# Kernel tuning notes

Hardware: AMD Instinct MI355X
Metric: run time of the kernel (lower is better)

## Reference

```python
import jax, jax.numpy as jnp
import numpy as np

N_HEAD = 16
D_HEAD = 64
MAX_REL = 512  # max_relative_positions


def setup_inputs() -> dict:
    key = jax.random.key(0)
    ks = jax.random.split(key, 9)
    B, S, D = 2, 2048, 1024
    return {
        "hidden_states": jax.random.normal(ks[0], (B, S, D), jnp.float32),
        "Wq": jax.random.normal(ks[1], (D, D), jnp.float32) * 0.02,
        "bq": jnp.zeros((D,), jnp.float32),
        "Wk": jax.random.normal(ks[2], (D, D), jnp.float32) * 0.02,
        "bk": jnp.zeros((D,), jnp.float32),
        "Wv": jax.random.normal(ks[3], (D, D), jnp.float32) * 0.02,
        "bv": jnp.zeros((D,), jnp.float32),
        "Wc": jax.random.normal(ks[4], (D, D), jnp.float32) * 0.02,
        "pos_table": jax.random.normal(ks[5], (2 * MAX_REL, D_HEAD), jnp.float32) * 0.02,
    }


def reference(hidden_states, Wq, bq, Wk, bk, Wv, bv, Wc, pos_table):
    B, S, D = hidden_states.shape
    H, Dh = N_HEAD, D_HEAD

    # QKV projections (torch Linear: x @ W.T + b)
    q = hidden_states @ Wq.T + bq
    k = hidden_states @ Wk.T + bk
    v = hidden_states @ Wv.T + bv
    q = q.reshape(B, S, H, Dh).transpose(0, 2, 1, 3)  # b h s d
    k = k.reshape(B, S, H, Dh).transpose(0, 2, 1, 3)
    v = v.reshape(B, S, H, Dh).transpose(0, 2, 1, 3)

    # relative position embedding lookup: [S, S, Dh]
    ar = jnp.arange(S)
    rel = jnp.clip(ar[:, None] - ar[None, :] + MAX_REL, 0, 2 * MAX_REL - 1)
    rpe = pos_table[rel]  # (S, S, Dh)

    # c2p: original einsum 'bhld,ijd->bhij' sums q over l (faithful)
    c2p = jnp.einsum('bhld,ijd->bhij', q, rpe)
    p2c = jnp.einsum('bhjd,ijd->bhij', k, jnp.flip(rpe, axis=0))
    bias = c2p + p2c  # (B, H, S, S)

    # SDPA with explicit attn_mask == bias added to scaled scores
    scale = 1.0 / jnp.sqrt(jnp.asarray(Dh, hidden_states.dtype))
    scores = jnp.einsum('bhid,bhjd->bhij', q, k) * scale + bias
    attn = jax.nn.softmax(scores, axis=-1)
    out = jnp.einsum('bhij,bhjd->bhid', attn, v)  # (B, H, S, Dh)

    out = out.transpose(0, 2, 1, 3).reshape(B, S, D)
    return out @ Wc.T  # c_proj has no bias; dropout is identity in eval
```

## Files before the change

kernel.cpp:

```cpp
#include <hip/hip_runtime.h>
#include <math.h>

#define BN   2
#define SEQ  2048
#define DIM  1024
#define NH   16
#define DH   64
#define TAB  1024
#define SCALE 0.125f
#define LOG2E 1.44269504088896340736f

typedef __attribute__((ext_vector_type(8))) short bf16x8;
typedef __attribute__((ext_vector_type(4))) float f32x4;

#if defined(__has_builtin)
#if __has_builtin(__builtin_amdgcn_exp2f)
#define EXP2F(x) __builtin_amdgcn_exp2f(x)
#else
#define EXP2F(x) exp2f(x)
#endif
#else
#define EXP2F(x) exp2f(x)
#endif

__device__ __forceinline__ short f2b(float f) {
    union { float f; unsigned u; } x; x.f = f;
    return (short)((x.u + 0x7fffu + ((x.u >> 16) & 1u)) >> 16);
}
__device__ __forceinline__ float b2f(short s) {
    union { float f; unsigned u; } x; x.u = ((unsigned)(unsigned short)s) << 16;
    return x.f;
}

#define GLDS16(gp, lp) __builtin_amdgcn_global_load_lds( \
    (const __attribute__((address_space(1))) void*)(gp), \
    (__attribute__((address_space(3))) void*)(lp), 16, 0, 0)

__device__ __forceinline__ bf16x8 fragS(const short* base, int row, int kq) {
    return *(const bf16x8*)(base + row * 64 + ((kq ^ (row & 7)) << 3));
}

__global__ __launch_bounds__(256) void f2b_multi_kernel(
    const float* __restrict__ s0, short* __restrict__ d0, int n0,
    const float* __restrict__ s1, short* __restrict__ d1,
    const float* __restrict__ s2, short* __restrict__ d2,
    const float* __restrict__ s3, short* __restrict__ d3, int nw,
    const float* __restrict__ s4, short* __restrict__ d4, int n4)
{
    const int z = blockIdx.z;
    const float* src = z == 0 ? s0 : (z == 1 ? s1 : (z == 2 ? s2 : (z == 3 ? s3 : s4)));
    short* dst       = z == 0 ? d0 : (z == 1 ? d1 : (z == 2 ? d2 : (z == 3 ? d3 : d4)));
    const int n      = z == 0 ? n0 : (z == 4 ? n4 : nw);
    int i = (blockIdx.x * 256 + threadIdx.x) * 8;
    if (i >= n) return;
    float4 a = *(const float4*)&src[i];
    float4 b = *(const float4*)&src[i + 4];
    bf16x8 o = { f2b(a.x), f2b(a.y), f2b(a.z), f2b(a.w),
                 f2b(b.x), f2b(b.y), f2b(b.z), f2b(b.w) };
    *(bf16x8*)&dst[i] = o;
}

__global__ __launch_bounds__(256) void qkv_mfma_kernel(
    const short* __restrict__ xb,
    const short* __restrict__ Wqb, const float* __restrict__ bq,
    const short* __restrict__ Wkb, const float* __restrict__ bk,
    const short* __restrict__ Wvb, const float* __restrict__ bv,
    short* __restrict__ q, short* __restrict__ k, short* __restrict__ v)
{
    const int which = blockIdx.z;
    const short* W    = which == 0 ? Wqb : (which == 1 ? Wkb : Wvb);
    const float* bias = which == 0 ? bq  : (which == 1 ? bk  : bv);
    short* outp       = which == 0 ? q   : (which == 1 ? k   : v);
    const float osc   = which == 0 ? SCALE * LOG2E : 1.0f;

    const int m0 = blockIdx.y * 128;
    const int n0 = blockIdx.x * 128;

    __shared__ short As[128 * 64];
    __shared__ short Bs[128 * 64];

    const int t  = threadIdx.x;
    const int w  = t >> 6;
    const int q4 = (t >> 4) & 3;
    const int l  = t & 15;
    const int wm = (w >> 1) * 64;
    const int wn = (w & 1) * 64;

    f32x4 acc[4][4];
#pragma unroll
    for (int mt = 0; mt < 4; ++mt)
#pragma unroll
        for (int nt = 0; nt < 4; ++nt) acc[mt][nt] = (f32x4){0.f,0.f,0.f,0.f};

    for (int k0 = 0; k0 < DIM; k0 += 64) {
        __syncthreads();
#pragma unroll
        for (int p = 0; p < 4; ++p) {
            const int cq = p * 256 + t;
            const int row = cq >> 3, bd = cq & 7;
            const int goff = (bd ^ (row & 7)) << 3;
            GLDS16(xb + (size_t)(m0 + row) * DIM + k0 + goff, As + cq * 8);
            GLDS16(W  + (size_t)(n0 + row) * DIM + k0 + goff, Bs + cq * 8);
        }
        __syncthreads();
#pragma unroll
        for (int kc = 0; kc < 2; ++kc) {
            bf16x8 af[4], bf[4];
#pragma unroll
            for (int mt = 0; mt < 4; ++mt) af[mt] = fragS(As, wm + mt*16 + l, kc*4 + q4);
#pragma unroll
            for (int nt = 0; nt < 4; ++nt) bf[nt] = fragS(Bs, wn + nt*16 + l, kc*4 + q4);
#pragma unroll
            for (int mt = 0; mt < 4; ++mt)
#pragma unroll
                for (int nt = 0; nt < 4; ++nt)
                    acc[mt][nt] = __builtin_amdgcn_mfma_f32_16x16x32_bf16(
                        af[mt], bf[nt], acc[mt][nt], 0, 0, 0);
        }
    }

    float bv4[4];
#pragma unroll
    for (int nt = 0; nt < 4; ++nt) bv4[nt] = bias[n0 + wn + nt*16 + l];
#pragma unroll
    for (int mt = 0; mt < 4; ++mt) {
#pragma unroll
        for (int r = 0; r < 4; ++r) {
            const int m  = m0 + wm + mt*16 + q4*4 + r;
            const int b_ = m >> 11, s_ = m & 2047;
#pragma unroll
            for (int nt = 0; nt < 4; ++nt) {
                const int o  = n0 + wn + nt*16 + l;
                const int h_ = o >> 6, d_ = o & 63;
                outp[((size_t)(b_*NH + h_) * SEQ + s_) * DH + d_] =
                    f2b((acc[mt][nt][r] + bv4[nt]) * osc);
            }
        }
    }
}

__global__ __launch_bounds__(256) void qsum_c2p_kernel(
    const short* __restrict__ q, const float* __restrict__ pt, float* __restrict__ c2p)
{
    const int bh = blockIdx.x;
    const short* qb = q + (size_t)bh * SEQ * DH;
    __shared__ float part[32][72];
    __shared__ float qs[64];
    const int t = threadIdx.x;
    const int dg = t & 7, sc = t >> 3;
    float a[8];
#pragma unroll
    for (int c = 0; c < 8; ++c) a[c] = 0.f;
    for (int s = sc * 64; s < sc * 64 + 64; ++s) {
        bf16x8 vv = *(const bf16x8*)&qb[(size_t)s * DH + dg * 8];
#pragma unroll
        for (int c = 0; c < 8; ++c) a[c] += b2f(vv[c]);
    }
#pragma unroll
    for (int c = 0; c < 8; ++c) part[sc][dg*8 + c] = a[c];
    __syncthreads();
    if (t < 64) {
        float s = 0.f;
#pragma unroll 8
        for (int i = 0; i < 32; ++i) s += part[i][t];
        qs[t] = s * 8.0f;
    }
    __syncthreads();
    for (int c = t; c < TAB; c += 256) {
        const float* ptr = pt + (size_t)c * DH;
        float s = 0.f;
#pragma unroll
        for (int dd = 0; dd < DH; dd += 4) {
            float4 p4 = *(const float4*)&ptr[dd];
            s += qs[dd]*p4.x + qs[dd+1]*p4.y + qs[dd+2]*p4.z + qs[dd+3]*p4.w;
        }
        c2p[(size_t)bh * TAB + c] = s;
    }
}

__global__ __launch_bounds__(256) void tgemm_kernel(
    const short* __restrict__ kglob, const short* __restrict__ ptb,
    short* __restrict__ slab, int bh0)
{
    const int G    = gridDim.z;
    const int gsub = G >> 3;
    const int fid  = (blockIdx.z * gridDim.y + blockIdx.y) * gridDim.x + blockIdx.x;
    const int g    = (fid & 7) * gsub + ((fid >> 3) % gsub);
    const int rest = fid / (8 * gsub);
    const int m0 = (rest >> 3) * 128;
    const int n0 = (rest & 7) * 128;

    const int bh = bh0 + g;
    const short* A = kglob + (size_t)bh * SEQ * DH;

    __shared__ short As[128 * 64];
    __shared__ short Bs[128 * 64];

    const int t  = threadIdx.x;
    const int w  = t >> 6;
    const int q4 = (t >> 4) & 3;
    const int l  = t & 15;
    const int wm = (w >> 1) * 64;
    const int wn = (w & 1) * 64;

#pragma unroll
    for (int p = 0; p < 4; ++p) {
        const int cq = p * 256 + t;
        const int row = cq >> 3, bd = cq & 7;
        const int go = (bd ^ (row & 7)) << 3;
        GLDS16(A   + (size_t)(m0 + row) * DH + go, As + cq * 8);
        GLDS16(ptb + (size_t)(n0 + row) * DH + go, Bs + cq * 8);
    }
    __syncthreads();

    f32x4 acc[4][4];
#pragma unroll
    for (int mt = 0; mt < 4; ++mt)
#pragma unroll
        for (int nt = 0; nt < 4; ++nt) acc[mt][nt] = (f32x4){0.f,0.f,0.f,0.f};
#pragma unroll
    for (int kc = 0; kc < 2; ++kc) {
        bf16x8 af[4], bf[4];
#pragma unroll
        for (int mt = 0; mt < 4; ++mt) af[mt] = fragS(As, wm + mt*16 + l, kc*4 + q4);
#pragma unroll
        for (int nt = 0; nt < 4; ++nt) bf[nt] = fragS(Bs, wn + nt*16 + l, kc*4 + q4);
#pragma unroll
        for (int mt = 0; mt < 4; ++mt)
#pragma unroll
            for (int nt = 0; nt < 4; ++nt)
                acc[mt][nt] = __builtin_amdgcn_mfma_f32_16x16x32_bf16(
                    af[mt], bf[nt], acc[mt][nt], 0, 0, 0);
    }

    short* outp = slab + (size_t)g * SEQ * 1024;
#pragma unroll
    for (int mt = 0; mt < 4; ++mt)
#pragma unroll
        for (int r = 0; r < 4; ++r) {
            const int m = m0 + wm + mt*16 + q4*4 + r;
#pragma unroll
            for (int nt = 0; nt < 4; ++nt)
                outp[(size_t)m * 1024 + n0 + wn + nt*16 + l] =
                    f2b(acc[mt][nt][r] * LOG2E);
        }
}

__global__ __launch_bounds__(256, 3) void attn_kernel(
    const short* __restrict__ q, const short* __restrict__ k, const short* __restrict__ v,
    const float* __restrict__ c2p, const short* __restrict__ slab,
    short* __restrict__ ao, int bh0)
{
    const int G    = gridDim.y;
    const int gsub = G >> 3;
    const int fid  = blockIdx.y * gridDim.x + blockIdx.x;
    const int g    = (fid & 7) * gsub + ((fid >> 3) % gsub);
    const int i0   = (fid / (8 * gsub)) * 64;

    const int bh = bh0 + g;
    const int b_ = bh >> 4, h_ = bh & 15;
    const short* qbh = q + (size_t)bh * SEQ * DH;
    const short* kbh = k + (size_t)bh * SEQ * DH;
    const short* vbh = v + (size_t)bh * SEQ * DH;
    const float* c2pb = c2p + (size_t)bh * TAB;
    const short* Tb   = slab + (size_t)g * SEQ * 1024;

    __shared__ short QsBand[64 * 72];
    __shared__ short Ks[64 * 64];
    __shared__ short Vt[64 * 64];
    __shared__ float cband[128];
    __shared__ float evf[64];

    const int t    = threadIdx.x;
    const int w    = t >> 6;
    const int q4   = (t >> 4) & 3;
    const int l    = t & 15;
    const int iLoc = w*16 + l;
    const int pq   = ((q4 & 1) << 1) | (q4 >> 1);

#pragma unroll
    for (int p = 0; p < 2; ++p) {
        const int cq = p * 256 + t;
        const int row = cq >> 3, bd = cq & 7;
        GLDS16(qbh + (size_t)(i0 + row) * DH + ((bd ^ (row & 7)) << 3), QsBand + cq * 8);
    }
    __syncthreads();
    const bf16x8 aq0 = fragS(QsBand, w*16 + l, q4);
    const bf16x8 aq1 = fragS(QsBand, w*16 + l, 4 + q4);

    float lsum = 0.f;
    f32x4 O[4];
#pragma unroll
    for (int dt = 0; dt < 4; ++dt) O[dt] = (f32x4){0.f, 0.f, 0.f, 0.f};

    const int jp  = t & 31;
    const int dgv = t >> 5;

    for (int j0 = 0; j0 < SEQ; j0 += 64) {
        const int Kc0 = 2559 - i0 - j0;
        const int cls = (Kc0 >= 1149) ? 0 : (Kc0 <= 0 ? 1 :
                        ((Kc0 >= 126 && Kc0 <= 1023) ? 2 : 3));
        __syncthreads();

#pragma unroll
        for (int p = 0; p < 2; ++p) {
            const int cq = p * 256 + t;
            const int row = cq >> 3, bd = cq & 7;
            GLDS16(kbh + (size_t)(j0 + row) * DH + ((bd ^ (row & 7)) << 3), Ks + cq * 8);
        }
        {
            const int j = 2 * jp, d0 = dgv * 8;
            bf16x8 va = *(const bf16x8*)(vbh + (size_t)(j0 + j)     * DH + d0);
            bf16x8 vb = *(const bf16x8*)(vbh + (size_t)(j0 + j + 1) * DH + d0);
#pragma unroll
            for (int c = 0; c < 8; ++c) {
                const int d = d0 + c;
                const int slot = d * 64 + (((j >> 3) ^ (d & 7)) << 3) + (j & 7);
                short2 pr; pr.x = va[c]; pr.y = vb[c];
                *(short2*)&Vt[slot] = pr;
            }
        }
        if (cls <= 1) {
            if (t < 64)
                evf[t] = b2f(Tb[(size_t)(j0 + t) * 1024 + (cls == 0 ? 1023 : 0)]);
        } else {
            const int rowj = t >> 2, m0b = t & 3;
            const int tb = Kc0 - rowj;
            const int af = min(max((tb - 63) & ~7, 0), 952);
            const short* srcrow = Tb + (size_t)(j0 + rowj) * 1024 + af;
            short* dstrow = &QsBand[rowj * 72];
            *(int4*)&dstrow[m0b * 8]       = *(const int4*)&srcrow[m0b * 8];
            *(int4*)&dstrow[(m0b + 4) * 8] = *(const int4*)&srcrow[(m0b + 4) * 8];
            if (m0b == 0)
                *(int4*)&dstrow[64] = *(const int4*)&srcrow[64];
        }
        if (t < 128) {
            int cc = min(max(449 + i0 - j0 + t, 0), TAB - 1);
            cband[t] = c2pb[cc];
        }
        __syncthreads();

        f32x4 st4[4];
        const int cb0 = iLoc - q4*4 + 63;
#pragma unroll
        for (int jt = 0; jt < 4; ++jt) {
            const int base = cb0 - jt*16;
            st4[jt][0] = cband[base];
            st4[jt][1] = cband[base - 1];
            st4[jt][2] = cband[base - 2];
            st4[jt][3] = cband[base - 3];
        }
        if (cls <= 1) {
#pragma unroll
            for (int jt = 0; jt < 4; ++jt) {
                const float4 e4 = *(const float4*)&evf[jt*16 + q4*4];
                st4[jt][0] += e4.x; st4[jt][1] += e4.y;
                st4[jt][2] += e4.z; st4[jt][3] += e4.w;
            }
        }

        __builtin_amdgcn_s_setprio(1);
#pragma unroll
        for (int jt = 0; jt < 4; ++jt) {
            bf16x8 a0 = fragS(Ks, jt*16 + l, q4);
            bf16x8 a1 = fragS(Ks, jt*16 + l, 4 + q4);
            st4[jt] = __builtin_amdgcn_mfma_f32_16x16x32_bf16(a0, aq0, st4[jt], 0, 0, 0);
            st4[jt] = __builtin_amdgcn_mfma_f32_16x16x32_bf16(a1, aq1, st4[jt], 0, 0, 0);
        }
        __builtin_amdgcn_s_setprio(0);

        float pv4[4][4];
        if (cls <= 1) {
#pragma unroll
            for (int jt = 0; jt < 4; ++jt)
#pragma unroll
                for (int r = 0; r < 4; ++r)
                    pv4[jt][r] = EXP2F(st4[jt][r]);
        } else if (cls == 2) {
#pragma unroll
            for (int jt = 0; jt < 4; ++jt)
#pragma unroll
                for (int r = 0; r < 4; ++r) {
                    const int jl = jt*16 + q4*4 + r;
                    const int tb = Kc0 - jl;
                    const int af = min((tb - 63) & ~7, 952);
                    pv4[jt][r] = EXP2F(st4[jt][r] +
                                       b2f(QsBand[jl * 72 + (tb - iLoc - af)]));
                }
        } else {
#pragma unroll
            for (int jt = 0; jt < 4; ++jt)
#pragma unroll
                for (int r = 0; r < 4; ++r) {
                    const int jl = jt*16 + q4*4 + r;
                    const int tb = Kc0 - jl;
                    const int af = min(max((tb - 63) & ~7, 0), 952);
                    const int y  = min(max(tb - iLoc, 0), 1023);
                    pv4[jt][r] = EXP2F(st4[jt][r] +
                                       b2f(QsBand[jl * 72 + (y - af)]));
                }
        }
#pragma unroll
        for (int jt = 0; jt < 4; ++jt)
#pragma unroll
            for (int r = 0; r < 4; ++r) lsum += pv4[jt][r];

        unsigned P2[4][2];
#pragma unroll
        for (int t2 = 0; t2 < 4; ++t2) {
            asm("v_cvt_pk_bf16_f32 %0, %1, %2"
                : "=v"(P2[t2][0]) : "v"(pv4[t2][0]), "v"(pv4[t2][1]));
            asm("v_cvt_pk_bf16_f32 %0, %1, %2"
                : "=v"(P2[t2][1]) : "v"(pv4[t2][2]), "v"(pv4[t2][3]));
        }
#pragma unroll
        for (int m = 0; m < 2; ++m) {
            asm("v_permlane16_swap_b32 %0, %1" : "+v"(P2[0][m]), "+v"(P2[1][m]));
            asm("v_permlane16_swap_b32 %0, %1" : "+v"(P2[2][m]), "+v"(P2[3][m]));
        }
        union { unsigned u[4]; bf16x8 v8; } UA, UB;
        UA.u[0] = P2[0][0]; UA.u[1] = P2[0][1]; UA.u[2] = P2[1][0]; UA.u[3] = P2[1][1];
        UB.u[0] = P2[2][0]; UB.u[1] = P2[2][1]; UB.u[2] = P2[3][0]; UB.u[3] = P2[3][1];

        __builtin_amdgcn_s_setprio(1);
#pragma unroll
        for (int dt = 0; dt < 4; ++dt) {
            bf16x8 b0 = fragS(Vt, dt*16 + l, pq);
            bf16x8 b1 = fragS(Vt, dt*16 + l, 4 + pq);
            O[dt] = __builtin_amdgcn_mfma_f32_16x16x32_bf16(UA.v8, b0, O[dt], 0, 0, 0);
            O[dt] = __builtin_amdgcn_mfma_f32_16x16x32_bf16(UB.v8, b1, O[dt], 0, 0, 0);
        }
        __builtin_amdgcn_s_setprio(0);
    }

    lsum += __shfl_xor(lsum, 16);
    lsum += __shfl_xor(lsum, 32);

#pragma unroll
    for (int r = 0; r < 4; ++r) {
        const float inv = 1.f / __shfl(lsum, q4*4 + r);
        const int i_g = i0 + w*16 + q4*4 + r;
        short* dst = ao + (((size_t)b_ * SEQ + i_g) * NH + h_) * DH + l;
#pragma unroll
        for (int dt = 0; dt < 4; ++dt)
            dst[dt*16] = f2b(O[dt][r] * inv);
    }
}

__global__ __launch_bounds__(256) void out_mfma_kernel(
    const short* __restrict__ xb, const float* __restrict__ W, float* __restrict__ out)
{
    const int m0 = blockIdx.y * 128;
    const int n0 = blockIdx.x * 128;

    __shared__ short As[128 * 64];
    __shared__ short Bs[128 * 64];

    const int t  = threadIdx.x;
    const int w  = t >> 6;
    const int q4 = (t >> 4) & 3;
    const int l  = t & 15;
    const int wm = (w >> 1) * 64;
    const int wn = (w & 1) * 64;

    f32x4 acc[4][4];
#pragma unroll
    for (int mt = 0; mt < 4; ++mt)
#pragma unroll
        for (int nt = 0; nt < 4; ++nt) acc[mt][nt] = (f32x4){0.f,0.f,0.f,0.f};

    for (int k0 = 0; k0 < DIM; k0 += 64) {
        __syncthreads();
#pragma unroll
        for (int p = 0; p < 4; ++p) {
            const int cq = p * 256 + t;
            const int row = cq >> 3, bd = cq & 7;
            GLDS16(xb + (size_t)(m0 + row) * DIM + k0 + ((bd ^ (row & 7)) << 3), As + cq * 8);
        }
        {
            const int row = t >> 1, h = t & 1;
#pragma unroll
            for (int c = 0; c < 4; ++c) {
                const int gch = h * 4 + c;
                const float* src = W + (size_t)(n0 + row) * DIM + k0 + gch * 8;
                float4 f0 = *(const float4*)src;
                float4 f1 = *(const float4*)(src + 4);
                bf16x8 o = { f2b(f0.x), f2b(f0.y), f2b(f0.z), f2b(f0.w),
                             f2b(f1.x), f2b(f1.y), f2b(f1.z), f2b(f1.w) };
                *(bf16x8*)&Bs[row * 64 + ((gch ^ (row & 7)) << 3)] = o;
            }
        }
        __syncthreads();
#pragma unroll
        for (int kc = 0; kc < 2; ++kc) {
            bf16x8 af[4], bf[4];
#pragma unroll
            for (int mt = 0; mt < 4; ++mt) af[mt] = fragS(As, wm + mt*16 + l, kc*4 + q4);
#pragma unroll
            for (int nt = 0; nt < 4; ++nt) bf[nt] = fragS(Bs, wn + nt*16 + l, kc*4 + q4);
#pragma unroll
            for (int mt = 0; mt < 4; ++mt)
#pragma unroll
                for (int nt = 0; nt < 4; ++nt)
                    acc[mt][nt] = __builtin_amdgcn_mfma_f32_16x16x32_bf16(
                        af[mt], bf[nt], acc[mt][nt], 0, 0, 0);
        }
    }
#pragma unroll
    for (int mt = 0; mt < 4; ++mt)
#pragma unroll
        for (int r = 0; r < 4; ++r) {
            const int m = m0 + wm + mt*16 + q4*4 + r;
#pragma unroll
            for (int nt = 0; nt < 4; ++nt)
                out[(size_t)m * DIM + n0 + wn + nt*16 + l] = acc[mt][nt][r];
        }
}

extern "C" void kernel_launch(void* const* d_in, const int* in_sizes, int n_in,
                              void* d_out, int out_size, void* d_ws, size_t ws_size,
                              hipStream_t stream)
{
    const float* hs = (const float*)d_in[0];
    const float* Wq = (const float*)d_in[1];
    const float* bq = (const float*)d_in[2];
    const float* Wk = (const float*)d_in[3];
    const float* bk = (const float*)d_in[4];
    const float* Wv = (const float*)d_in[5];
    const float* bv = (const float*)d_in[6];
    const float* Wc = (const float*)d_in[7];
    const float* pt = (const float*)d_in[8];
    float* out = (float*)d_out;

    const size_t XE    = (size_t)BN * SEQ * DIM;
    const size_t WE    = (size_t)DIM * DIM;
    const size_t PE    = (size_t)TAB * DH;
    const size_t SLAB1 = (size_t)SEQ * 1024;

    short* sw   = (short*)d_ws;
    short* qb   = sw;
    short* kb   = sw + XE;
    short* vb   = sw + 2 * XE;
    short* aob  = sw + 3 * XE;
    float* c2p  = (float*)(sw + 4 * XE);
    short* ptb  = sw + 4 * XE + 65536;
    short* slab = sw + 4 * XE + 65536 + PE;
    short* xb   = slab;
    short* wqb  = slab + XE;
    short* wkb  = wqb + WE;
    short* wvb  = wkb + WE;

    const size_t fixed_sh = 4 * XE + 65536 + PE;
    const size_t avail_sh = (ws_size / 2 > fixed_sh) ? ws_size / 2 - fixed_sh : 0;
    const int G = (avail_sh >= 32 * SLAB1) ? 32 : ((avail_sh >= 16 * SLAB1) ? 16 : 8);

    f2b_multi_kernel<<<dim3((int)(XE/2048), 1, 5), 256, 0, stream>>>(
        hs, xb, (int)XE, Wq, wqb, Wk, wkb, Wv, wvb, (int)WE, pt, ptb, (int)PE);

    qkv_mfma_kernel<<<dim3(DIM/128, (BN*SEQ)/128, 3), 256, 0, stream>>>(
        xb, wqb, bq, wkb, bk, wvb, bv, qb, kb, vb);

    qsum_c2p_kernel<<<dim3(BN*NH), 256, 0, stream>>>(qb, pt, c2p);

    for (int bh0 = 0; bh0 < BN*NH; bh0 += G) {
        tgemm_kernel<<<dim3(1024/128, SEQ/128, G), 256, 0, stream>>>(kb, ptb, slab, bh0);
        attn_kernel<<<dim3(SEQ/64, G), 256, 0, stream>>>(qb, kb, vb, c2p, slab, aob, bh0);
    }

    out_mfma_kernel<<<dim3(DIM/128, (BN*SEQ)/128), 256, 0, stream>>>(aob, Wc, out);
}
```

Baseline: 341.2 us.

## Double-buffer K, V, bias band and c2p tiles in the attention loop

The attention kernel gets ping-pong LDS buffers for K, the transposed V, the relative-position band, the c2p band and the edge values. The next tile's global loads are issued into registers, or straight into LDS via GLDS16, before computing on the current tile, and are written to the other buffer after the PV MFMAs. This drops one barrier per iteration and is meant to hide global-load latency behind the MFMA and exp work. In exchange it roughly doubles LDS use and holds more live registers, which may reduce occupancy.

```diff
diff --git a/kernel.cpp b/kernel.cpp
--- a/kernel.cpp
+++ b/kernel.cpp
@@ -265,11 +265,12 @@
     const float* c2pb = c2p + (size_t)bh * TAB;
     const short* Tb   = slab + (size_t)g * SEQ * 1024;
 
-    __shared__ short QsBand[64 * 72];
-    __shared__ short Ks[64 * 64];
-    __shared__ short Vt[64 * 64];
-    __shared__ float cband[128];
-    __shared__ float evf[64];
+    __shared__ short BandA[64 * 72];
+    __shared__ short BandB[64 * 72];
+    __shared__ short KsA[64 * 64], KsB[64 * 64];
+    __shared__ short VtA[64 * 64], VtB[64 * 64];
+    __shared__ float cbA[128], cbB[128];
+    __shared__ float evA[64], evB[64];
 
     const int t    = threadIdx.x;
     const int w    = t >> 6;
@@ -278,82 +279,140 @@
     const int iLoc = w*16 + l;
     const int pq   = ((q4 & 1) << 1) | (q4 >> 1);
 
+    const int jp  = t & 31;
+    const int dgv = t >> 5;
+    const int rowj = t >> 2, m0b = t & 3;
+
 #pragma unroll
     for (int p = 0; p < 2; ++p) {
         const int cq = p * 256 + t;
         const int row = cq >> 3, bd = cq & 7;
-        GLDS16(qbh + (size_t)(i0 + row) * DH + ((bd ^ (row & 7)) << 3), QsBand + cq * 8);
+        GLDS16(qbh + (size_t)(i0 + row) * DH + ((bd ^ (row & 7)) << 3), BandA + cq * 8);
     }
     __syncthreads();
-    const bf16x8 aq0 = fragS(QsBand, w*16 + l, q4);
-    const bf16x8 aq1 = fragS(QsBand, w*16 + l, 4 + q4);
-
-    float lsum = 0.f;
-    f32x4 O[4];
-#pragma unroll
-    for (int dt = 0; dt < 4; ++dt) O[dt] = (f32x4){0.f, 0.f, 0.f, 0.f};
-
-    const int jp  = t & 31;
-    const int dgv = t >> 5;
-
-    for (int j0 = 0; j0 < SEQ; j0 += 64) {
-        const int Kc0 = 2559 - i0 - j0;
-        const int cls = (Kc0 >= 1149) ? 0 : (Kc0 <= 0 ? 1 :
-                        ((Kc0 >= 126 && Kc0 <= 1023) ? 2 : 3));
-        __syncthreads();
-
+    const bf16x8 aq0 = fragS(BandA, w*16 + l, q4);
+    const bf16x8 aq1 = fragS(BandA, w*16 + l, 4 + q4);
+    __syncthreads();
+
+    {
+        const int j0n = 0;
+        const int Kc0n = 2559 - i0;
+        const int clsn = (Kc0n >= 1149) ? 0 : (Kc0n <= 0 ? 1 :
+                         ((Kc0n >= 126 && Kc0n <= 1023) ? 2 : 3));
 #pragma unroll
         for (int p = 0; p < 2; ++p) {
             const int cq = p * 256 + t;
             const int row = cq >> 3, bd = cq & 7;
-            GLDS16(kbh + (size_t)(j0 + row) * DH + ((bd ^ (row & 7)) << 3), Ks + cq * 8);
+            GLDS16(kbh + (size_t)(j0n + row) * DH + ((bd ^ (row & 7)) << 3), KsA + cq * 8);
         }
         {
-            const int j = 2 * jp, d0 = dgv * 8;
-            bf16x8 va = *(const bf16x8*)(vbh + (size_t)(j0 + j)     * DH + d0);
-            bf16x8 vb = *(const bf16x8*)(vbh + (size_t)(j0 + j + 1) * DH + d0);
+            const int jv = 2 * jp, d0v = dgv * 8;
+            bf16x8 va = *(const bf16x8*)(vbh + (size_t)(j0n + jv)     * DH + d0v);
+            bf16x8 vb = *(const bf16x8*)(vbh + (size_t)(j0n + jv + 1) * DH + d0v);
 #pragma unroll
             for (int c = 0; c < 8; ++c) {
-                const int d = d0 + c;
-                const int slot = d * 64 + (((j >> 3) ^ (d & 7)) << 3) + (j & 7);
+                const int d = d0v + c;
+                const int slot = d * 64 + (((jv >> 3) ^ (d & 7)) << 3) + (jv & 7);
                 short2 pr; pr.x = va[c]; pr.y = vb[c];
-                *(short2*)&Vt[slot] = pr;
-            }
-        }
-        if (cls <= 1) {
+                *(short2*)&VtA[slot] = pr;
+            }
+        }
+        if (clsn <= 1) {
             if (t < 64)
-                evf[t] = b2f(Tb[(size_t)(j0 + t) * 1024 + (cls == 0 ? 1023 : 0)]);
+                evA[t] = b2f(Tb[(size_t)(j0n + t) * 1024 + (clsn == 0 ? 1023 : 0)]);
         } else {
-            const int rowj = t >> 2, m0b = t & 3;
-            const int tb = Kc0 - rowj;
+            const int tb = Kc0n - rowj;
             const int af = min(max((tb - 63) & ~7, 0), 952);
-            const short* srcrow = Tb + (size_t)(j0 + rowj) * 1024 + af;
-            short* dstrow = &QsBand[rowj * 72];
+            const short* srcrow = Tb + (size_t)(j0n + rowj) * 1024 + af;
+            short* dstrow = &BandA[rowj * 72];
             *(int4*)&dstrow[m0b * 8]       = *(const int4*)&srcrow[m0b * 8];
             *(int4*)&dstrow[(m0b + 4) * 8] = *(const int4*)&srcrow[(m0b + 4) * 8];
             if (m0b == 0)
                 *(int4*)&dstrow[64] = *(const int4*)&srcrow[64];
         }
         if (t < 128) {
-            int cc = min(max(449 + i0 - j0 + t, 0), TAB - 1);
-            cband[t] = c2pb[cc];
-        }
-        __syncthreads();
+            int cc = min(max(449 + i0 - j0n + t, 0), TAB - 1);
+            cbA[t] = c2pb[cc];
+        }
+    }
+    __syncthreads();
+
+    float lsum = 0.f;
+    f32x4 O[4];
+#pragma unroll
+    for (int dt = 0; dt < 4; ++dt) O[dt] = (f32x4){0.f, 0.f, 0.f, 0.f};
+
+    for (int it = 0; it < 32; ++it) {
+        const int j0  = it * 64;
+        const int par = it & 1;
+        const short* KsC   = par ? KsB   : KsA;
+        const short* VtC   = par ? VtB   : VtA;
+        const short* BandC = par ? BandB : BandA;
+        const float* cbC   = par ? cbB   : cbA;
+        const float* evC   = par ? evB   : evA;
+        short* KsN   = par ? KsA   : KsB;
+        short* VtN   = par ? VtA   : VtB;
+        short* BandN = par ? BandA : BandB;
+        float* cbN   = par ? cbA   : cbB;
+        float* evN   = par ? evA   : evB;
+
+        const int Kc0 = 2559 - i0 - j0;
+        const int cls = (Kc0 >= 1149) ? 0 : (Kc0 <= 0 ? 1 :
+                        ((Kc0 >= 126 && Kc0 <= 1023) ? 2 : 3));
+
+        const bool have_nxt = (it < 31);
+        const int j0n  = j0 + 64;
+        const int Kc0n = Kc0 - 64;
+        const int clsn = (Kc0n >= 1149) ? 0 : (Kc0n <= 0 ? 1 :
+                         ((Kc0n >= 126 && Kc0n <= 1023) ? 2 : 3));
+
+        bf16x8 va = {}, vb = {};
+        int4 bl0 = {}, bl1 = {}, bl2 = {};
+        float cbv = 0.f, evv = 0.f;
+        int afn = 0;
+        if (have_nxt) {
+#pragma unroll
+            for (int p = 0; p < 2; ++p) {
+                const int cq = p * 256 + t;
+                const int row = cq >> 3, bd = cq & 7;
+                GLDS16(kbh + (size_t)(j0n + row) * DH + ((bd ^ (row & 7)) << 3), KsN + cq * 8);
+            }
+            {
+                const int jv = 2 * jp, d0v = dgv * 8;
+                va = *(const bf16x8*)(vbh + (size_t)(j0n + jv)     * DH + d0v);
+                vb = *(const bf16x8*)(vbh + (size_t)(j0n + jv + 1) * DH + d0v);
+            }
+            if (clsn <= 1) {
+                if (t < 64)
+                    evv = b2f(Tb[(size_t)(j0n + t) * 1024 + (clsn == 0 ? 1023 : 0)]);
+            } else {
+                const int tb = Kc0n - rowj;
+                afn = min(max((tb - 63) & ~7, 0), 952);
+                const short* srcrow = Tb + (size_t)(j0n + rowj) * 1024 + afn;
+                bl0 = *(const int4*)&srcrow[m0b * 8];
+                bl1 = *(const int4*)&srcrow[(m0b + 4) * 8];
+                if (m0b == 0) bl2 = *(const int4*)&srcrow[64];
+            }
+            if (t < 128) {
+                int cc = min(max(449 + i0 - j0n + t, 0), TAB - 1);
+                cbv = c2pb[cc];
+            }
+        }
 
         f32x4 st4[4];
         const int cb0 = iLoc - q4*4 + 63;
 #pragma unroll
         for (int jt = 0; jt < 4; ++jt) {
             const int base = cb0 - jt*16;
-            st4[jt][0] = cband[base];
-            st4[jt][1] = cband[base - 1];
-            st4[jt][2] = cband[base - 2];
-            st4[jt][3] = cband[base - 3];
+            st4[jt][0] = cbC[base];
+            st4[jt][1] = cbC[base - 1];
+            st4[jt][2] = cbC[base - 2];
+            st4[jt][3] = cbC[base - 3];
         }
         if (cls <= 1) {
 #pragma unroll
             for (int jt = 0; jt < 4; ++jt) {
-                const float4 e4 = *(const float4*)&evf[jt*16 + q4*4];
+                const float4 e4 = *(const float4*)&evC[jt*16 + q4*4];
                 st4[jt][0] += e4.x; st4[jt][1] += e4.y;
                 st4[jt][2] += e4.z; st4[jt][3] += e4.w;
             }
@@ -362,8 +421,8 @@
         __builtin_amdgcn_s_setprio(1);
 #pragma unroll
         for (int jt = 0; jt < 4; ++jt) {
-            bf16x8 a0 = fragS(Ks, jt*16 + l, q4);
-            bf16x8 a1 = fragS(Ks, jt*16 + l, 4 + q4);
+            bf16x8 a0 = fragS(KsC, jt*16 + l, q4);
+            bf16x8 a1 = fragS(KsC, jt*16 + l, 4 + q4);
             st4[jt] = __builtin_amdgcn_mfma_f32_16x16x32_bf16(a0, aq0, st4[jt], 0, 0, 0);
             st4[jt] = __builtin_amdgcn_mfma_f32_16x16x32_bf16(a1, aq1, st4[jt], 0, 0, 0);
         }
@@ -385,7 +444,7 @@
                     const int tb = Kc0 - jl;
                     const int af = min((tb - 63) & ~7, 952);
                     pv4[jt][r] = EXP2F(st4[jt][r] +
-                                       b2f(QsBand[jl * 72 + (tb - iLoc - af)]));
+                                       b2f(BandC[jl * 72 + (tb - iLoc - af)]));
                 }
         } else {
 #pragma unroll
@@ -397,7 +456,7 @@
                     const int af = min(max((tb - 63) & ~7, 0), 952);
                     const int y  = min(max(tb - iLoc, 0), 1023);
                     pv4[jt][r] = EXP2F(st4[jt][r] +
-                                       b2f(QsBand[jl * 72 + (y - af)]));
+                                       b2f(BandC[jl * 72 + (y - af)]));
                 }
         }
 #pragma unroll
@@ -425,12 +484,35 @@
         __builtin_amdgcn_s_setprio(1);
 #pragma unroll
         for (int dt = 0; dt < 4; ++dt) {
-            bf16x8 b0 = fragS(Vt, dt*16 + l, pq);
-            bf16x8 b1 = fragS(Vt, dt*16 + l, 4 + pq);
+            bf16x8 b0 = fragS(VtC, dt*16 + l, pq);
+            bf16x8 b1 = fragS(VtC, dt*16 + l, 4 + pq);
             O[dt] = __builtin_amdgcn_mfma_f32_16x16x32_bf16(UA.v8, b0, O[dt], 0, 0, 0);
             O[dt] = __builtin_amdgcn_mfma_f32_16x16x32_bf16(UB.v8, b1, O[dt], 0, 0, 0);
         }
         __builtin_amdgcn_s_setprio(0);
+
+        if (have_nxt) {
+            {
+                const int jv = 2 * jp, d0v = dgv * 8;
+#pragma unroll
+                for (int c = 0; c < 8; ++c) {
+                    const int d = d0v + c;
+                    const int slot = d * 64 + (((jv >> 3) ^ (d & 7)) << 3) + (jv & 7);
+                    short2 pr; pr.x = va[c]; pr.y = vb[c];
+                    *(short2*)&VtN[slot] = pr;
+                }
+            }
+            if (clsn <= 1) {
+                if (t < 64) evN[t] = evv;
+            } else {
+                short* dstrow = &BandN[rowj * 72];
+                *(int4*)&dstrow[m0b * 8]       = bl0;
+                *(int4*)&dstrow[(m0b + 4) * 8] = bl1;
+                if (m0b == 0) *(int4*)&dstrow[64] = bl2;
+            }
+            if (t < 128) cbN[t] = cbv;
+        }
+        __syncthreads();
     }
 
     lsum += __shfl_xor(lsum, 16);
```

New measurement: 350.8 us. +2.8%, slower.

## Read bias band and c2p directly from global instead of staging in LDS

Applied to the files above, without the earlier changes.

Drops the LDS staging of the positional slab band, the c2p band and the edge vector, along with the per-tile case classification. Each thread now gathers its 16 bias terms straight from global memory with clamped indices, and Q is staged through the K buffer to save LDS. The intent is to cut LDS footprint, barriers and branch divergence. In exchange it issues scattered, uncoalesced 2-byte global loads with a stride of a 2KB row per element, which adds latency inside the main loop.

```diff
diff --git a/kernel.cpp b/kernel.cpp
--- a/kernel.cpp
+++ b/kernel.cpp
@@ -265,11 +265,8 @@
     const float* c2pb = c2p + (size_t)bh * TAB;
     const short* Tb   = slab + (size_t)g * SEQ * 1024;
 
-    __shared__ short QsBand[64 * 72];
     __shared__ short Ks[64 * 64];
     __shared__ short Vt[64 * 64];
-    __shared__ float cband[128];
-    __shared__ float evf[64];
 
     const int t    = threadIdx.x;
     const int w    = t >> 6;
@@ -278,29 +275,27 @@
     const int iLoc = w*16 + l;
     const int pq   = ((q4 & 1) << 1) | (q4 >> 1);
 
+    const int jp  = t & 31;
+    const int dgv = t >> 5;
+
 #pragma unroll
     for (int p = 0; p < 2; ++p) {
         const int cq = p * 256 + t;
         const int row = cq >> 3, bd = cq & 7;
-        GLDS16(qbh + (size_t)(i0 + row) * DH + ((bd ^ (row & 7)) << 3), QsBand + cq * 8);
+        GLDS16(qbh + (size_t)(i0 + row) * DH + ((bd ^ (row & 7)) << 3), Ks + cq * 8);
     }
     __syncthreads();
-    const bf16x8 aq0 = fragS(QsBand, w*16 + l, q4);
-    const bf16x8 aq1 = fragS(QsBand, w*16 + l, 4 + q4);
+    const bf16x8 aq0 = fragS(Ks, w*16 + l, q4);
+    const bf16x8 aq1 = fragS(Ks, w*16 + l, 4 + q4);
+    __syncthreads();
 
     float lsum = 0.f;
     f32x4 O[4];
 #pragma unroll
     for (int dt = 0; dt < 4; ++dt) O[dt] = (f32x4){0.f, 0.f, 0.f, 0.f};
 
-    const int jp  = t & 31;
-    const int dgv = t >> 5;
-
     for (int j0 = 0; j0 < SEQ; j0 += 64) {
         const int Kc0 = 2559 - i0 - j0;
-        const int cls = (Kc0 >= 1149) ? 0 : (Kc0 <= 0 ? 1 :
-                        ((Kc0 >= 126 && Kc0 <= 1023) ? 2 : 3));
-        __syncthreads();
 
 #pragma unroll
         for (int p = 0; p < 2; ++p) {
@@ -320,44 +315,27 @@
                 *(short2*)&Vt[slot] = pr;
             }
         }
-        if (cls <= 1) {
-            if (t < 64)
-                evf[t] = b2f(Tb[(size_t)(j0 + t) * 1024 + (cls == 0 ? 1023 : 0)]);
-        } else {
-            const int rowj = t >> 2, m0b = t & 3;
-            const int tb = Kc0 - rowj;
-            const int af = min(max((tb - 63) & ~7, 0), 952);
-            const short* srcrow = Tb + (size_t)(j0 + rowj) * 1024 + af;
-            short* dstrow = &QsBand[rowj * 72];
-            *(int4*)&dstrow[m0b * 8]       = *(const int4*)&srcrow[m0b * 8];
-            *(int4*)&dstrow[(m0b + 4) * 8] = *(const int4*)&srcrow[(m0b + 4) * 8];
-            if (m0b == 0)
-                *(int4*)&dstrow[64] = *(const int4*)&srcrow[64];
-        }
-        if (t < 128) {
-            int cc = min(max(449 + i0 - j0 + t, 0), TAB - 1);
-            cband[t] = c2pb[cc];
-        }
         __syncthreads();
 
         f32x4 st4[4];
-        const int cb0 = iLoc - q4*4 + 63;
-#pragma unroll
-        for (int jt = 0; jt < 4; ++jt) {
-            const int base = cb0 - jt*16;
-            st4[jt][0] = cband[base];
-            st4[jt][1] = cband[base - 1];
-            st4[jt][2] = cband[base - 2];
-            st4[jt][3] = cband[base - 3];
-        }
-        if (cls <= 1) {
-#pragma unroll
-            for (int jt = 0; jt < 4; ++jt) {
-                const float4 e4 = *(const float4*)&evf[jt*16 + q4*4];
-                st4[jt][0] += e4.x; st4[jt][1] += e4.y;
-                st4[jt][2] += e4.z; st4[jt][3] += e4.w;
+        const int ccb = 512 + i0 + iLoc - j0;
+#pragma unroll
+        for (int jt = 0; jt < 4; ++jt)
+#pragma unroll
+            for (int r = 0; r < 4; ++r) {
+                const int jl = jt*16 + q4*4 + r;
+                st4[jt][r] = c2pb[min(max(ccb - jl, 0), TAB - 1)];
             }
-        }
+
+        short tband[16];
+#pragma unroll
+        for (int jt = 0; jt < 4; ++jt)
+#pragma unroll
+            for (int r = 0; r < 4; ++r) {
+                const int jl = jt*16 + q4*4 + r;
+                const int y  = min(max(Kc0 - jl - iLoc, 0), TAB - 1);
+                tband[jt*4 + r] = Tb[(size_t)(j0 + jl) * 1024 + y];
+            }
 
         __builtin_amdgcn_s_setprio(1);
 #pragma unroll
@@ -370,40 +348,13 @@
         __builtin_amdgcn_s_setprio(0);
 
         float pv4[4][4];
-        if (cls <= 1) {
-#pragma unroll
-            for (int jt = 0; jt < 4; ++jt)
-#pragma unroll
-                for (int r = 0; r < 4; ++r)
-                    pv4[jt][r] = EXP2F(st4[jt][r]);
-        } else if (cls == 2) {
-#pragma unroll
-            for (int jt = 0; jt < 4; ++jt)
-#pragma unroll
-                for (int r = 0; r < 4; ++r) {
-                    const int jl = jt*16 + q4*4 + r;
-                    const int tb = Kc0 - jl;
-                    const int af = min((tb - 63) & ~7, 952);
-                    pv4[jt][r] = EXP2F(st4[jt][r] +
-                                       b2f(QsBand[jl * 72 + (tb - iLoc - af)]));
-                }
-        } else {
-#pragma unroll
-            for (int jt = 0; jt < 4; ++jt)
-#pragma unroll
-                for (int r = 0; r < 4; ++r) {
-                    const int jl = jt*16 + q4*4 + r;
-                    const int tb = Kc0 - jl;
-                    const int af = min(max((tb - 63) & ~7, 0), 952);
-                    const int y  = min(max(tb - iLoc, 0), 1023);
-                    pv4[jt][r] = EXP2F(st4[jt][r] +
-                                       b2f(QsBand[jl * 72 + (y - af)]));
-                }
-        }
 #pragma unroll
         for (int jt = 0; jt < 4; ++jt)
 #pragma unroll
-            for (int r = 0; r < 4; ++r) lsum += pv4[jt][r];
+            for (int r = 0; r < 4; ++r) {
+                pv4[jt][r] = EXP2F(st4[jt][r] + b2f(tband[jt*4 + r]));
+                lsum += pv4[jt][r];
+            }
 
         unsigned P2[4][2];
 #pragma unroll
@@ -431,6 +382,7 @@
             O[dt] = __builtin_amdgcn_mfma_f32_16x16x32_bf16(UB.v8, b1, O[dt], 0, 0, 0);
         }
         __builtin_amdgcn_s_setprio(0);
+        __syncthreads();
     }
 
     lsum += __shfl_xor(lsum, 16);
```

Result: faster. 308.9 us (-9.5%).
